# Kernel tuning notes

Hardware: AMD Instinct MI355X
Metric: run time of the kernel (lower is better)

## Reference

```python
import jax, jax.numpy as jnp
import numpy as np
from jax import lax


def setup_inputs() -> dict:
    key = jax.random.key(0)
    ks = jax.random.split(key, 6)
    B, T, F, C = 32, 256, 64, 16
    CO, P, S, K = 16, 64, 32, 4
    x = jax.random.normal(ks[0], (B, T, F, C), dtype=jnp.float32)
    static = jax.random.normal(ks[1], (B, S), dtype=jnp.float32)
    conv_w = jax.random.normal(ks[2], (F, CO, C, K), dtype=jnp.float32) * (1.0 / np.sqrt(C * K))
    conv_b = jax.random.normal(ks[3], (F, CO), dtype=jnp.float32) * 0.01
    W_p = jax.random.normal(ks[4], (F * C + S, P), dtype=jnp.float32) * (1.0 / np.sqrt(F * C + S))
    b_p = jax.random.normal(ks[5], (P,), dtype=jnp.float32) * 0.01
    return {"x": x, "static": static, "conv_w": conv_w, "conv_b": conv_b,
            "W_p": W_p, "b_p": b_p, "dilation": 2}


def _tpc_forward(x, static, conv_w, conv_b, W_p, b_p, dilation):
    B, T, F, C = x.shape
    _, CO, _, K = conv_w.shape
    left_pad = dilation * (K - 1)
    # --- feature-wise causal temporal conv as one grouped dilated conv ---
    # [B, T, F, C] -> [B, F*C, T]  (NCH layout)
    xr = x.transpose(0, 2, 3, 1).reshape(B, F * C, T)
    kr = conv_w.reshape(F * CO, C, K)  # groups = F
    y = lax.conv_general_dilated(
        xr, kr,
        window_strides=(1,),
        padding=[(left_pad, 0)],  # causal left padding
        rhs_dilation=(dilation,),
        dimension_numbers=("NCH", "OIH", "NCH"),
        feature_group_count=F,
    )  # [B, F*CO, T]
    temp_out = y.reshape(B, F, CO, T).transpose(0, 3, 1, 2) + conv_b[None, None, :, :]
    # --- pointwise branch on flattened features + static ---
    flat_x = x.reshape(B, T, F * C)
    static_rep = jnp.broadcast_to(static[:, None, :], (B, T, static.shape[-1]))
    point_in = jnp.concatenate([flat_x, static_rep], axis=-1)  # [B, T, F*C+S]
    point_out = point_in @ W_p + b_p  # [B, T, P]
    point_bcast = jnp.broadcast_to(point_out[:, :, None, :], (B, T, F, point_out.shape[-1]))
    # --- concat fusion + ReLU ---
    fused = jnp.concatenate([x, temp_out, point_bcast], axis=-1)
    return jax.nn.relu(fused)


def reference(x, static, conv_w, conv_b, W_p, b_p, dilation):
    return _tpc_forward(x, static, conv_w, conv_b, W_p, b_p, dilation)
```

## Files before the change

kernel.cpp:

```cpp
#include <hip/hip_runtime.h>

#define B_  32
#define T_  256
#define F_  64
#define C_  16
#define CO_ 16
#define P_  64
#define S_  32
#define K_  4
#define FC_ 1024
#define OUTC 96

__global__ __launch_bounds__(256) void point_gemm(
    const float* __restrict__ x, const float* __restrict__ stat,
    const float* __restrict__ Wp, const float* __restrict__ bp,
    float* __restrict__ pout)
{
    int tid = threadIdx.x;
    int tx  = tid & 63;
    int ty  = tid >> 6;
    int blk = blockIdx.x;
    int b   = blk >> 4;
    int t0  = (blk & 15) << 4;
    int row0 = t0 + ty * 4;

    float sacc = bp[tx];
    const float* wst = Wp + (size_t)FC_ * P_;
    #pragma unroll 8
    for (int s = 0; s < S_; ++s)
        sacc += stat[b * S_ + s] * wst[s * P_ + tx];

    float acc0 = sacc, acc1 = sacc, acc2 = sacc, acc3 = sacc;
    const float* xrow = x + ((size_t)(b * T_ + row0)) * FC_;
    for (int k0 = 0; k0 < FC_; k0 += 4) {
        float b0 = Wp[(size_t)(k0 + 0) * P_ + tx];
        float b1 = Wp[(size_t)(k0 + 1) * P_ + tx];
        float b2 = Wp[(size_t)(k0 + 2) * P_ + tx];
        float b3 = Wp[(size_t)(k0 + 3) * P_ + tx];
        float4 x0 = *(const float4*)(xrow + 0 * FC_ + k0);
        float4 x1 = *(const float4*)(xrow + 1 * FC_ + k0);
        float4 x2 = *(const float4*)(xrow + 2 * FC_ + k0);
        float4 x3 = *(const float4*)(xrow + 3 * FC_ + k0);
        acc0 += x0.x * b0 + x0.y * b1 + x0.z * b2 + x0.w * b3;
        acc1 += x1.x * b0 + x1.y * b1 + x1.z * b2 + x1.w * b3;
        acc2 += x2.x * b0 + x2.y * b1 + x2.z * b2 + x2.w * b3;
        acc3 += x3.x * b0 + x3.y * b1 + x3.z * b2 + x3.w * b3;
    }
    float* orow = pout + ((size_t)(b * T_ + row0)) * P_ + tx;
    orow[0 * P_] = acc0;
    orow[1 * P_] = acc1;
    orow[2 * P_] = acc2;
    orow[3 * P_] = acc3;
}

__global__ __launch_bounds__(256) void fuse_conv(
    const float* __restrict__ x, const float* __restrict__ cw,
    const float* __restrict__ cb, const float* __restrict__ pnt,
    float* __restrict__ out)
{
    __shared__ __align__(16) float xs[38 * 256];
    int tid = threadIdx.x;
    int blk = blockIdx.x;
    int b   = blk >> 5;
    int r   = blk & 31;
    int t0  = (r >> 2) * 32;
    int f0  = (r & 3) * 16;
    int f_loc = tid >> 4;
    int co    = tid & 15;
    int f     = f0 + f_loc;

    for (int it = 0; it < 10; ++it) {
        int v = it * 256 + tid;
        if (v < 38 * 64) {
            int slice = v >> 6;
            int pos   = v & 63;
            int tg    = t0 - 6 + slice;
            float4 val = make_float4(0.f, 0.f, 0.f, 0.f);
            if (tg >= 0)
                val = *(const float4*)(x + ((size_t)(b * T_ + tg) * F_ + f0) * C_ + pos * 4);
            *(float4*)(xs + slice * 256 + pos * 4) = val;
        }
    }

    float w[64];
    const float4* wg = (const float4*)(cw + ((size_t)(f * CO_ + co)) * (C_ * K_));
    #pragma unroll
    for (int j = 0; j < 16; ++j) {
        float4 v = wg[j];
        w[j * 4 + 0] = v.x; w[j * 4 + 1] = v.y;
        w[j * 4 + 2] = v.z; w[j * 4 + 3] = v.w;
    }
    float bias = cb[f * CO_ + co];

    __syncthreads();

    int lane = tid & 63;
    int g0   = tid >> 6;

    for (int tl = 0; tl < 32; ++tl) {
        int t = t0 + tl;
        float temp = bias;
        #pragma unroll
        for (int k = 0; k < K_; ++k) {
            const float* sp = xs + (tl + 2 * k) * 256 + f_loc * 16;
            #pragma unroll
            for (int c4 = 0; c4 < 4; ++c4) {
                float4 xv = *(const float4*)(sp + c4 * 4);
                temp += xv.x * w[(c4 * 4 + 0) * 4 + k];
                temp += xv.y * w[(c4 * 4 + 1) * 4 + k];
                temp += xv.z * w[(c4 * 4 + 2) * 4 + k];
                temp += xv.w * w[(c4 * 4 + 3) * 4 + k];
            }
        }
        float* ob = out + ((size_t)(b * T_ + t) * F_ + f0) * OUTC;
        ob[f_loc * OUTC + 16 + co] = fmaxf(temp, 0.f);
        ob[f_loc * OUTC + co] = fmaxf(xs[(tl + 6) * 256 + f_loc * 16 + co], 0.f);
        float pv = fmaxf(pnt[((size_t)(b * T_ + t)) * P_ + lane], 0.f);
        #pragma unroll
        for (int g = 0; g < 4; ++g) {
            int fl = g * 4 + g0;
            ob[fl * OUTC + 32 + lane] = pv;
        }
    }
}

extern "C" void kernel_launch(void* const* d_in, const int* in_sizes, int n_in,
                              void* d_out, int out_size, void* d_ws, size_t ws_size,
                              hipStream_t stream) {
    const float* x    = (const float*)d_in[0];
    const float* stat = (const float*)d_in[1];
    const float* cw   = (const float*)d_in[2];
    const float* cb   = (const float*)d_in[3];
    const float* Wp   = (const float*)d_in[4];
    const float* bp   = (const float*)d_in[5];
    float* out = (float*)d_out;
    float* pnt = (float*)d_ws;

    point_gemm<<<512, 256, 0, stream>>>(x, stat, Wp, bp, pnt);
    fuse_conv<<<1024, 256, 0, stream>>>(x, cw, cb, pnt, out);
}
```

Measured before the change: 339.9 us.

## Fuse pointwise GEMM and temporal conv into a single kernel

Merges the pointwise GEMM and the conv/concat kernel into one launch. Each block handles all 64 features for 8 timesteps, staging the x rows in shared memory once and reusing them for both the GEMM (split-K across 8 warps, reduced through shared memory) and the dilated conv. This removes the workspace round trip for the point output and the second launch. In exchange, each block reloads W_p, which increases redundant weight reads, uses more shared memory per block, and loads 14 rows to produce 8 outputs, so halo overhead is higher.

```diff
diff --git a/kernel.cpp b/kernel.cpp
--- a/kernel.cpp
+++ b/kernel.cpp
@@ -10,117 +10,122 @@
 #define K_  4
 #define FC_ 1024
 #define OUTC 96
+#define TT  8
+#define NS  14
 
-__global__ __launch_bounds__(256) void point_gemm(
+__global__ __launch_bounds__(512, 4) void tpc_fused(
     const float* __restrict__ x, const float* __restrict__ stat,
+    const float* __restrict__ cw, const float* __restrict__ cb,
     const float* __restrict__ Wp, const float* __restrict__ bp,
-    float* __restrict__ pout)
-{
-    int tid = threadIdx.x;
-    int tx  = tid & 63;
-    int ty  = tid >> 6;
-    int blk = blockIdx.x;
-    int b   = blk >> 4;
-    int t0  = (blk & 15) << 4;
-    int row0 = t0 + ty * 4;
-
-    float sacc = bp[tx];
-    const float* wst = Wp + (size_t)FC_ * P_;
-    #pragma unroll 8
-    for (int s = 0; s < S_; ++s)
-        sacc += stat[b * S_ + s] * wst[s * P_ + tx];
-
-    float acc0 = sacc, acc1 = sacc, acc2 = sacc, acc3 = sacc;
-    const float* xrow = x + ((size_t)(b * T_ + row0)) * FC_;
-    for (int k0 = 0; k0 < FC_; k0 += 4) {
-        float b0 = Wp[(size_t)(k0 + 0) * P_ + tx];
-        float b1 = Wp[(size_t)(k0 + 1) * P_ + tx];
-        float b2 = Wp[(size_t)(k0 + 2) * P_ + tx];
-        float b3 = Wp[(size_t)(k0 + 3) * P_ + tx];
-        float4 x0 = *(const float4*)(xrow + 0 * FC_ + k0);
-        float4 x1 = *(const float4*)(xrow + 1 * FC_ + k0);
-        float4 x2 = *(const float4*)(xrow + 2 * FC_ + k0);
-        float4 x3 = *(const float4*)(xrow + 3 * FC_ + k0);
-        acc0 += x0.x * b0 + x0.y * b1 + x0.z * b2 + x0.w * b3;
-        acc1 += x1.x * b0 + x1.y * b1 + x1.z * b2 + x1.w * b3;
-        acc2 += x2.x * b0 + x2.y * b1 + x2.z * b2 + x2.w * b3;
-        acc3 += x3.x * b0 + x3.y * b1 + x3.z * b2 + x3.w * b3;
-    }
-    float* orow = pout + ((size_t)(b * T_ + row0)) * P_ + tx;
-    orow[0 * P_] = acc0;
-    orow[1 * P_] = acc1;
-    orow[2 * P_] = acc2;
-    orow[3 * P_] = acc3;
-}
-
-__global__ __launch_bounds__(256) void fuse_conv(
-    const float* __restrict__ x, const float* __restrict__ cw,
-    const float* __restrict__ cb, const float* __restrict__ pnt,
     float* __restrict__ out)
 {
-    __shared__ __align__(16) float xs[38 * 256];
+    __shared__ __align__(16) float xs[NS * FC_];
+    __shared__ __align__(16) float part[8 * TT * P_];
+    __shared__ __align__(16) float pout[TT * P_];
+
     int tid = threadIdx.x;
     int blk = blockIdx.x;
-    int b   = blk >> 5;
-    int r   = blk & 31;
-    int t0  = (r >> 2) * 32;
-    int f0  = (r & 3) * 16;
-    int f_loc = tid >> 4;
-    int co    = tid & 15;
-    int f     = f0 + f_loc;
+    int b  = blk >> 5;
+    int t0 = (blk & 31) * TT;
 
-    for (int it = 0; it < 10; ++it) {
-        int v = it * 256 + tid;
-        if (v < 38 * 64) {
-            int slice = v >> 6;
-            int pos   = v & 63;
-            int tg    = t0 - 6 + slice;
-            float4 val = make_float4(0.f, 0.f, 0.f, 0.f);
-            if (tg >= 0)
-                val = *(const float4*)(x + ((size_t)(b * T_ + tg) * F_ + f0) * C_ + pos * 4);
-            *(float4*)(xs + slice * 256 + pos * 4) = val;
+    #pragma unroll
+    for (int it = 0; it < 7; ++it) {
+        int v = it * 512 + tid;
+        int slice = v >> 8;
+        int pos   = v & 255;
+        int tg = t0 - 6 + slice;
+        float4 val = make_float4(0.f, 0.f, 0.f, 0.f);
+        if (tg >= 0)
+            val = *(const float4*)(x + ((size_t)(b * T_ + tg)) * FC_ + pos * 4);
+        *(float4*)(xs + slice * FC_ + pos * 4) = val;
+    }
+    __syncthreads();
+
+    {
+        int p  = tid & 63;
+        int ks = tid >> 6;
+        float acc[TT];
+        #pragma unroll
+        for (int r = 0; r < TT; ++r) acc[r] = 0.f;
+        int k0base = ks * 128;
+        for (int kk = 0; kk < 128; kk += 4) {
+            int k0 = k0base + kk;
+            float w0 = Wp[(size_t)(k0 + 0) * P_ + p];
+            float w1 = Wp[(size_t)(k0 + 1) * P_ + p];
+            float w2 = Wp[(size_t)(k0 + 2) * P_ + p];
+            float w3 = Wp[(size_t)(k0 + 3) * P_ + p];
+            #pragma unroll
+            for (int r = 0; r < TT; ++r) {
+                float4 xv = *(const float4*)(xs + (6 + r) * FC_ + k0);
+                acc[r] += xv.x * w0 + xv.y * w1 + xv.z * w2 + xv.w * w3;
+            }
+        }
+        #pragma unroll
+        for (int r = 0; r < TT; ++r)
+            part[(ks * TT + r) * P_ + p] = acc[r];
+    }
+    __syncthreads();
+
+    {
+        int p = tid & 63;
+        int r = tid >> 6;
+        float s = bp[p];
+        const float* wst = Wp + (size_t)FC_ * P_;
+        #pragma unroll 8
+        for (int si = 0; si < S_; ++si)
+            s += stat[b * S_ + si] * wst[si * P_ + p];
+        #pragma unroll
+        for (int ks = 0; ks < 8; ++ks)
+            s += part[(ks * TT + r) * P_ + p];
+        pout[r * P_ + p] = fmaxf(s, 0.f);
+    }
+    __syncthreads();
+
+    int p  = tid & 63;
+    int fg = tid >> 6;
+    float pv[TT];
+    #pragma unroll
+    for (int r = 0; r < TT; ++r) pv[r] = pout[r * P_ + p];
+
+    int co = tid & 15;
+    int fh = tid >> 4;
+    #pragma unroll
+    for (int half = 0; half < 2; ++half) {
+        int f = fh + half * 32;
+        float w[64];
+        const float4* wg = (const float4*)(cw + ((size_t)(f * CO_ + co)) * (C_ * K_));
+        #pragma unroll
+        for (int j = 0; j < 16; ++j) {
+            float4 t4 = wg[j];
+            w[4 * j + 0] = t4.x; w[4 * j + 1] = t4.y;
+            w[4 * j + 2] = t4.z; w[4 * j + 3] = t4.w;
+        }
+        float bias = cb[f * CO_ + co];
+        for (int tl = 0; tl < TT; ++tl) {
+            float temp = bias;
+            #pragma unroll
+            for (int k = 0; k < K_; ++k) {
+                const float* sp = xs + (tl + 2 * k) * FC_ + f * C_;
+                #pragma unroll
+                for (int c4 = 0; c4 < 4; ++c4) {
+                    float4 xv = *(const float4*)(sp + c4 * 4);
+                    temp += xv.x * w[(c4 * 4 + 0) * 4 + k];
+                    temp += xv.y * w[(c4 * 4 + 1) * 4 + k];
+                    temp += xv.z * w[(c4 * 4 + 2) * 4 + k];
+                    temp += xv.w * w[(c4 * 4 + 3) * 4 + k];
+                }
+            }
+            float* ob = out + ((size_t)(b * T_ + t0 + tl)) * F_ * OUTC;
+            ob[f * OUTC + 16 + co] = fmaxf(temp, 0.f);
+            ob[f * OUTC + co] = fmaxf(xs[(tl + 6) * FC_ + f * C_ + co], 0.f);
         }
     }
-
-    float w[64];
-    const float4* wg = (const float4*)(cw + ((size_t)(f * CO_ + co)) * (C_ * K_));
-    #pragma unroll
-    for (int j = 0; j < 16; ++j) {
-        float4 v = wg[j];
-        w[j * 4 + 0] = v.x; w[j * 4 + 1] = v.y;
-        w[j * 4 + 2] = v.z; w[j * 4 + 3] = v.w;
-    }
-    float bias = cb[f * CO_ + co];
-
-    __syncthreads();
-
-    int lane = tid & 63;
-    int g0   = tid >> 6;
-
-    for (int tl = 0; tl < 32; ++tl) {
-        int t = t0 + tl;
-        float temp = bias;
+    for (int tl = 0; tl < TT; ++tl) {
+        float* ob = out + ((size_t)(b * T_ + t0 + tl)) * F_ * OUTC + 32 + p;
+        float val = pv[tl];
         #pragma unroll
-        for (int k = 0; k < K_; ++k) {
-            const float* sp = xs + (tl + 2 * k) * 256 + f_loc * 16;
-            #pragma unroll
-            for (int c4 = 0; c4 < 4; ++c4) {
-                float4 xv = *(const float4*)(sp + c4 * 4);
-                temp += xv.x * w[(c4 * 4 + 0) * 4 + k];
-                temp += xv.y * w[(c4 * 4 + 1) * 4 + k];
-                temp += xv.z * w[(c4 * 4 + 2) * 4 + k];
-                temp += xv.w * w[(c4 * 4 + 3) * 4 + k];
-            }
-        }
-        float* ob = out + ((size_t)(b * T_ + t) * F_ + f0) * OUTC;
-        ob[f_loc * OUTC + 16 + co] = fmaxf(temp, 0.f);
-        ob[f_loc * OUTC + co] = fmaxf(xs[(tl + 6) * 256 + f_loc * 16 + co], 0.f);
-        float pv = fmaxf(pnt[((size_t)(b * T_ + t)) * P_ + lane], 0.f);
-        #pragma unroll
-        for (int g = 0; g < 4; ++g) {
-            int fl = g * 4 + g0;
-            ob[fl * OUTC + 32 + lane] = pv;
-        }
+        for (int fo = 0; fo < 8; ++fo)
+            ob[(fo * 8 + fg) * OUTC] = val;
     }
 }
 
@@ -134,8 +139,6 @@
     const float* Wp   = (const float*)d_in[4];
     const float* bp   = (const float*)d_in[5];
     float* out = (float*)d_out;
-    float* pnt = (float*)d_ws;
 
-    point_gemm<<<512, 256, 0, stream>>>(x, stat, Wp, bp, pnt);
-    fuse_conv<<<1024, 256, 0, stream>>>(x, cw, cb, pnt, out);
+    tpc_fused<<<1024, 512, 0, stream>>>(x, stat, cw, cb, Wp, bp, out);
 }
```

Result: slower. 389.8 us (+14.7%).
